# Kernel tuning notes

Hardware: AMD Instinct MI355X
Metric: run time of the kernel (lower is better)

## Reference

```python
import jax, jax.numpy as jnp
import numpy as np
from jax import lax


def _lstm_cell(x, h, c, W_ih, W_hh, b_ih, b_hh):
    # torch nn.LSTMCell: gates = x W_ih^T + b_ih + h W_hh^T + b_hh, order i,f,g,o
    gates = x @ W_ih.T + h @ W_hh.T + (b_ih + b_hh)
    i, f, g, o = jnp.split(gates, 4, axis=-1)
    c_new = jax.nn.sigmoid(f) * c + jax.nn.sigmoid(i) * jnp.tanh(g)
    h_new = jax.nn.sigmoid(o) * jnp.tanh(c_new)
    return h_new, c_new


def setup_inputs():
    key = jax.random.key(0)
    ks = jax.random.split(key, 10)
    B, S, E, H, V = 128, 20, 512, 512, 10000
    images = jax.random.normal(ks[0], (B, E), jnp.float32)
    captions = jax.random.randint(ks[1], (B, S), 0, V)
    length = jax.random.randint(ks[2], (B, 1), 2, S + 1)
    length = length.at[0, 0].set(S)  # guarantee max decode length == S-1 (static shape)
    s = 0.05
    emb = jax.random.normal(ks[3], (V, E), jnp.float32) * s
    W_ih = jax.random.normal(ks[4], (4 * H, E), jnp.float32) * s
    W_hh = jax.random.normal(ks[5], (4 * H, H), jnp.float32) * s
    b_ih = jax.random.normal(ks[6], (4 * H,), jnp.float32) * s
    b_hh = jax.random.normal(ks[7], (4 * H,), jnp.float32) * s
    fc_w = jax.random.normal(ks[8], (V, H), jnp.float32) * s
    fc_b = jax.random.normal(ks[9], (V,), jnp.float32) * s
    return dict(images=images, captions=captions, length=length, emb=emb,
                W_ih=W_ih, W_hh=W_hh, b_ih=b_ih, b_hh=b_hh, fc_w=fc_w, fc_b=fc_b)


def reference(images, captions, length, emb, W_ih, W_hh, b_ih, b_hh, fc_w, fc_b):
    B, S = captions.shape
    T = S - 1  # static max(decode_lengths) by construction
    H = W_hh.shape[1]
    lens = length[:, 0]
    sort_ind = jnp.argsort(-lens)  # stable descending sort, like torch .sort(descending=True)
    sorted_lens = lens[sort_ind]
    dec_len = sorted_lens - 1
    features = images[sort_ind]
    captions_s = captions[sort_ind]
    embeddings = emb[captions_s]  # [B, S, E]

    zeros = jnp.zeros((B, H), images.dtype)
    h, c = _lstm_cell(features, zeros, zeros, W_ih, W_hh, b_ih, b_hh)

    xs = (jnp.swapaxes(embeddings[:, :T, :], 0, 1), jnp.arange(T))  # [T,B,E], [T]

    def step(carry, x):
        h, c = carry
        x_t, t = x
        # ragged batch in the original == masking here: rows with dec_len<=t never
        # contribute to any future valid output (lengths sorted descending).
        h, c = _lstm_cell(x_t, h, c, W_ih, W_hh, b_ih, b_hh)
        preds = h @ fc_w.T + fc_b  # dropout is identity in eval mode
        preds = jnp.where((dec_len > t)[:, None], preds, 0.0)
        return (h, c), preds

    (_, _), preds = lax.scan(step, (h, c), xs)
    predictions = jnp.swapaxes(preds, 0, 1)  # [B, T, V]
    return predictions, captions_s, dec_len, sort_ind
```

## Files before the change

### kernel.cpp

```cpp
#include <hip/hip_runtime.h>

typedef float  f32x4 __attribute__((ext_vector_type(4)));
typedef short  s16x8 __attribute__((ext_vector_type(8)));
typedef unsigned short u16x4 __attribute__((ext_vector_type(4)));

#define MFMA16(a,b,c) __builtin_amdgcn_mfma_f32_16x16x32_bf16(a,b,c,0,0,0)

#define PRED_ELEMS 24320000ull

__device__ __forceinline__ unsigned short f2bf(float f){
  unsigned u = __builtin_bit_cast(unsigned, f);
  u += 0x7fffu + ((u >> 16) & 1u);
  return (unsigned short)(u >> 16);
}
__device__ __forceinline__ float sigf(float x){ return 1.0f/(1.0f + __expf(-x)); }
__device__ __forceinline__ float tanh_(float x){
  x = fminf(15.0f, fmaxf(-15.0f, x));
  float e = __expf(2.0f*x);
  return (e - 1.0f) / (e + 1.0f);
}
__device__ __forceinline__ s16x8 ld8(const unsigned short* p){
  return *reinterpret_cast<const s16x8*>(p);
}
__device__ __forceinline__ void gload_lds16(const unsigned short* src, unsigned short* dst){
  __builtin_amdgcn_global_load_lds(
      (const __attribute__((address_space(1))) void*)src,
      (__attribute__((address_space(3))) void*)dst, 16, 0, 0);
}

__global__ void k0_sort(const int* __restrict__ length, const int* __restrict__ captions,
                        float* __restrict__ out, int* __restrict__ sortp,
                        int* __restrict__ nactp, unsigned int* __restrict__ cnt4k)
{
  __shared__ int sl[128], sdl[128], ssi[128];
  int tid = threadIdx.x;
  for (int k = tid; k < 1024; k += 128) cnt4k[k] = 0u;
  if (tid < 128) sl[tid] = length[tid];
  __syncthreads();
  if (tid < 128){
    int l = sl[tid];
    int rank = 0;
    for (int j = 0; j < 128; ++j){
      int lj = sl[j];
      rank += (lj > l) || (lj == l && j < tid);
    }
    sortp[rank] = tid;
    ssi[rank] = tid;   sdl[rank] = l - 1;
  }
  __syncthreads();
  if (tid < 20){
    int c = 0;
    for (int r = 0; r < 128; ++r) c += (sdl[r] >= tid);
    nactp[tid] = c;
  }
  if (tid < 128){
    const size_t P = PRED_ELEMS;
    int si = ssi[tid];
    for (int t = 0; t < 20; ++t) out[P + tid*20 + t] = (float)captions[si*20 + t];
    out[P + 2560 + tid] = (float)sdl[tid];
    out[P + 2688 + tid] = (float)si;
  }
}

__device__ __forceinline__ void cvt4(unsigned short* dst, const float* src, int u){
  f32x4 v = *reinterpret_cast<const f32x4*>(src + (size_t)u*4);
  u16x4 o;
  o[0]=f2bf(v[0]); o[1]=f2bf(v[1]); o[2]=f2bf(v[2]); o[3]=f2bf(v[3]);
  *reinterpret_cast<u16x4*>(dst + (size_t)u*4) = o;
}

__global__ void k1_convert(const float* __restrict__ images, const int* __restrict__ captions,
    const float* __restrict__ emb, const float* __restrict__ wih, const float* __restrict__ whh,
    const float* __restrict__ bih, const float* __restrict__ bhh, const float* __restrict__ fcw,
    const int* __restrict__ sortp,
    unsigned short* __restrict__ wihb, unsigned short* __restrict__ whhb,
    unsigned short* __restrict__ fcwb, float* __restrict__ biasp,
    unsigned short* __restrict__ xseq, unsigned short* __restrict__ hseq,
    unsigned short* __restrict__ hloc)
{
  const int U0 = 262144;
  const int U1 = 262144;
  const int U2 = 1294336;
  const int U3 = 512;
  const int U4 = 327680;
  const int U5 = 16384;
  const int U6 = 16384;
  const int total = U0+U1+U2+U3+U4+U5+U6;
  for (int i = blockIdx.x*blockDim.x + threadIdx.x; i < total; i += gridDim.x*blockDim.x){
    int j = i;
    if (j < U0){ cvt4(wihb, wih, j); continue; }
    j -= U0;
    if (j < U1){ cvt4(whhb, whh, j); continue; }
    j -= U1;
    if (j < U2){
      int row = j >> 7;
      if (row < 10000) cvt4(fcwb, fcw, j);
      else { u16x4 z = {0,0,0,0}; *reinterpret_cast<u16x4*>(fcwb + (size_t)j*4) = z; }
      continue;
    }
    j -= U2;
    if (j < U3){
      int e0 = j*4;
      for (int e = 0; e < 4; ++e) biasp[e0+e] = bih[e0+e] + bhh[e0+e];
      continue;
    }
    j -= U3;
    if (j < U4){
      int elem = j*4;
      int s = elem >> 16;
      int rem = elem & 65535;
      int r = rem >> 9;
      int k = rem & 511;
      const float* src;
      if (s == 0) src = images + (size_t)sortp[r]*512 + k;
      else {
        int cap = captions[sortp[r]*20 + (s-1)];
        src = emb + (size_t)cap*512 + k;
      }
      f32x4 v = *reinterpret_cast<const f32x4*>(src);
      u16x4 o;
      o[0]=f2bf(v[0]); o[1]=f2bf(v[1]); o[2]=f2bf(v[2]); o[3]=f2bf(v[3]);
      *reinterpret_cast<u16x4*>(xseq + (size_t)j*4) = o;
      continue;
    }
    j -= U4;
    if (j < U5){ u16x4 z = {0,0,0,0}; *reinterpret_cast<u16x4*>(hseq + (size_t)j*4) = z; continue; }
    j -= U5;
    {
      int e0 = j*4;
      int x = e0 >> 13;
      int rem = e0 & 8191;
      u16x4 z = {0,0,0,0};
      *reinterpret_cast<u16x4*>(hloc + (size_t)x*172032 + rem) = z;
    }
  }
}

__global__ __launch_bounds__(256) void lstm_chain(
    const unsigned short* __restrict__ xseq, const unsigned short* __restrict__ wih,
    const unsigned short* __restrict__ whh, const float* __restrict__ biasp,
    unsigned short* __restrict__ hseq, unsigned short* __restrict__ hloc,
    const int* __restrict__ nact, unsigned int* __restrict__ claimc,
    unsigned int* __restrict__ flags)
{
  const int tid = threadIdx.x;
  __shared__ int s_xw;
  __shared__ unsigned short WIl[64*524];
  __shared__ unsigned short WHl[64*524];
  __shared__ float pg[4][4][16][17];

  if (tid == 0){
    unsigned xcc;
    asm volatile("s_getreg_b32 %0, hwreg(20, 0, 4)" : "=s"(xcc));
    int x = (int)(xcc & 7u);
    unsigned slot = __hip_atomic_fetch_add(claimc + x*64, 1u,
                      __ATOMIC_RELAXED, __HIP_MEMORY_SCOPE_AGENT);
    s_xw = (x << 8) | (int)(slot & 255u);
  }
  __syncthreads();
  const int x = s_xw >> 8;
  const int w = s_xw & 255;
  if (w >= 32) return;
  const int R0 = x*16;
  const int C0 = w*16;
  unsigned int* myflags = flags + x*64;

  const int lane = tid & 63;
  const int kk   = tid >> 6;
  const int fr   = lane & 15;
  const int fkq  = (lane >> 4) * 8;

  for (int idx = tid; idx < 64*64; idx += 256){
    int lr = idx >> 6, kc = (idx & 63)*8;
    int q = lr >> 4, jj = lr & 15;
    size_t off = (size_t)(q*512 + C0 + jj)*512 + kc;
    *reinterpret_cast<s16x8*>(&WIl[lr*524 + kc]) = ld8(wih + off);
    *reinterpret_cast<s16x8*>(&WHl[lr*524 + kc]) = ld8(whh + off);
  }

  unsigned short* hl = hloc + (size_t)x*172032;
  const int prow = tid >> 4;
  const int pcol = tid & 15;
  const float bz0 = biasp[       C0 + pcol];
  const float bz1 = biasp[ 512 + C0 + pcol];
  const float bz2 = biasp[1024 + C0 + pcol];
  const float bz3 = biasp[1536 + C0 + pcol];
  float creg = 0.f;

  s16x8 ax[4];
  #pragma unroll
  for (int i = 0; i < 4; ++i)
    ax[i] = ld8(xseq + (R0 + fr)*512 + kk*128 + i*32 + fkq);
  __syncthreads();

  for (int s = 0; s < 20; ++s){
    if (R0 >= nact[s]) break;
    const unsigned short* hp = hl + (size_t)s*8192;

    s16x8 ah[4];
    #pragma unroll
    for (int i = 0; i < 4; ++i)
      ah[i] = ld8(hp + fr*512 + kk*128 + i*32 + fkq);

    #pragma unroll
    for (int q = 0; q < 4; ++q){
      f32x4 accx = (f32x4){0.f,0.f,0.f,0.f};
      f32x4 acch = (f32x4){0.f,0.f,0.f,0.f};
      #pragma unroll
      for (int i = 0; i < 4; ++i){
        s16x8 bi = *reinterpret_cast<const s16x8*>(&WIl[(q*16 + fr)*524 + kk*128 + i*32 + fkq]);
        accx = MFMA16(ax[i], bi, accx);
      }
      #pragma unroll
      for (int i = 0; i < 4; ++i){
        s16x8 bh = *reinterpret_cast<const s16x8*>(&WHl[(q*16 + fr)*524 + kk*128 + i*32 + fkq]);
        acch = MFMA16(ah[i], bh, acch);
      }
      const int rr = (lane >> 4) * 4;
      #pragma unroll
      for (int p = 0; p < 4; ++p)
        pg[kk][q][rr + p][fr] = accx[p] + acch[p];
    }
    __syncthreads();

    unsigned short hb;
    {
      float iv = pg[0][0][prow][pcol] + pg[1][0][prow][pcol]
               + pg[2][0][prow][pcol] + pg[3][0][prow][pcol] + bz0;
      float fv = pg[0][1][prow][pcol] + pg[1][1][prow][pcol]
               + pg[2][1][prow][pcol] + pg[3][1][prow][pcol] + bz1;
      float gv = pg[0][2][prow][pcol] + pg[1][2][prow][pcol]
               + pg[2][2][prow][pcol] + pg[3][2][prow][pcol] + bz2;
      float ov = pg[0][3][prow][pcol] + pg[1][3][prow][pcol]
               + pg[2][3][prow][pcol] + pg[3][3][prow][pcol] + bz3;
      creg = sigf(fv)*creg + sigf(iv)*tanh_(gv);
      float h = sigf(ov)*tanh_(creg);
      hb = f2bf(h);
      hl[(size_t)(s+1)*8192 + prow*512 + C0 + pcol] = hb;
    }
    __syncthreads();

    hseq[(size_t)(s+1)*65536 + (R0 + prow)*512 + C0 + pcol] = hb;

    if (s < 19 && nact[s+1] > R0){
      const unsigned tgt = (unsigned)(s + 1);
      const unsigned short* xp = xseq + (size_t)(s+1)*65536;
      #pragma unroll
      for (int i = 0; i < 4; ++i)
        ax[i] = ld8(xp + (R0 + fr)*512 + kk*128 + i*32 + fkq);

      if (tid == 0){
        unsigned int* fa = myflags + w;
        asm volatile("global_atomic_swap %0, %1, off"
                     :: "v"(fa), "v"(tgt) : "memory");
      }
      if (tid < 64){
        unsigned int* pa = myflags + (tid & 31);
        long guard = 0;
        for (;;){
          bool ok = true;
          if (tid < 32){
            unsigned old;
            asm volatile("global_atomic_add %0, %1, %2, off sc0\n\t"
                         "s_waitcnt vmcnt(0)"
                         : "=v"(old) : "v"(pa), "v"(0u) : "memory");
            ok = (old >= tgt);
          }
          if (__all(ok) || ++guard > (1L << 20)) break;
          __builtin_amdgcn_s_sleep(1);
        }
      }
      __syncthreads();
    }
  }
}

__global__ __launch_bounds__(256) void fc_kernel(
    const unsigned short* __restrict__ hseq, const unsigned short* __restrict__ fcwb,
    const float* __restrict__ fcb, const int* __restrict__ nact,
    float* __restrict__ out)
{
  const int b    = blockIdx.x;
  const int x    = b & 7;
  const int slot = b >> 3;
  const int t    = slot % 19;
  const int p    = x + 8*(slot/19);
  if (p >= 79) return;
  const int v0   = p * 128;
  const int tid  = threadIdx.x;

  __shared__ unsigned short Ab[2][128*64];
  __shared__ unsigned short Bb[2][128*64];

  const unsigned short* Ag = hseq + (size_t)(t + 2)*65536;
  const unsigned short* Bg = fcwb + (size_t)v0*512;
  const int n_t = nact[t + 1];

  const int srow = tid >> 3;
  const int sphy = tid & 7;
  const int wuni = (tid >> 6) << 9;

  #define STAGE(gsrc, lbuf, kt)                                              \
    _Pragma("unroll")                                                        \
    for (int call = 0; call < 4; ++call){                                    \
      int row_ = call*32 + srow;                                             \
      gload_lds16(gsrc + (size_t)row_*512 + (kt)*64 + ((sphy ^ (row_ & 7)) << 3), \
                  lbuf + call*2048 + wuni);                                  \
    }

  const int lane = tid & 63;
  const int wv   = tid >> 6;
  const int wr   = wv >> 1, wc = wv & 1;
  const int fr   = lane & 15;
  const int hi   = lane >> 4;

  f32x4 acc[4][4];
  #pragma unroll
  for (int i = 0; i < 4; ++i)
    #pragma unroll
    for (int j = 0; j < 4; ++j)
      acc[i][j] = (f32x4){0.f,0.f,0.f,0.f};

  STAGE(Ag, Ab[0], 0)
  STAGE(Bg, Bb[0], 0)
  asm volatile("s_waitcnt vmcnt(0)" ::: "memory");
  __syncthreads();

  int cur = 0;
  for (int kt = 0; kt < 8; ++kt){
    if (kt < 7){
      STAGE(Ag, Ab[cur^1], kt+1)
      STAGE(Bg, Bb[cur^1], kt+1)
    }
    const unsigned short* As = Ab[cur];
    const unsigned short* Bs = Bb[cur];
    #pragma unroll
    for (int kk = 0; kk < 2; ++kk){
      const int c = kk*4 + hi;
      s16x8 af[4], bf[4];
      #pragma unroll
      for (int i = 0; i < 4; ++i){
        int row = wr*64 + i*16 + fr;
        af[i] = ld8(As + row*64 + ((c ^ (row & 7)) << 3));
      }
      #pragma unroll
      for (int j = 0; j < 4; ++j){
        int col = wc*64 + j*16 + fr;
        bf[j] = ld8(Bs + col*64 + ((c ^ (col & 7)) << 3));
      }
      #pragma unroll
      for (int i = 0; i < 4; ++i)
        #pragma unroll
        for (int j = 0; j < 4; ++j)
          acc[i][j] = MFMA16(af[i], bf[j], acc[i][j]);
    }
    asm volatile("s_waitcnt vmcnt(0)" ::: "memory");
    __syncthreads();
    cur ^= 1;
  }

  const int rr = hi * 4;
  #pragma unroll
  for (int j = 0; j < 4; ++j){
    int v = v0 + wc*64 + j*16 + fr;
    if (v >= 10000) continue;
    float bb = fcb[v];
    #pragma unroll
    for (int i = 0; i < 4; ++i){
      #pragma unroll
      for (int pp = 0; pp < 4; ++pp){
        int r = wr*64 + i*16 + rr + pp;
        out[(size_t)(r*19 + t)*10000 + v] = (r < n_t) ? (acc[i][j][pp] + bb) : 0.0f;
      }
    }
  }
  #undef STAGE
}

extern "C" void kernel_launch(void* const* d_in, const int* in_sizes, int n_in,
                              void* d_out, int out_size, void* d_ws, size_t ws_size,
                              hipStream_t stream) {
  const float* images   = (const float*)d_in[0];
  const int*   captions = (const int*)  d_in[1];
  const int*   length   = (const int*)  d_in[2];
  const float* emb      = (const float*)d_in[3];
  const float* W_ih     = (const float*)d_in[4];
  const float* W_hh     = (const float*)d_in[5];
  const float* b_ih     = (const float*)d_in[6];
  const float* b_hh     = (const float*)d_in[7];
  const float* fc_w     = (const float*)d_in[8];
  const float* fc_b     = (const float*)d_in[9];
  float* out = (float*)d_out;
  char*  ws  = (char*)d_ws;

  int*            sortp  = (int*)           (ws + 0);
  int*            nactp  = (int*)           (ws + 2048);
  float*          biasp  = (float*)         (ws + 4096);
  unsigned int*   cnt4k  = (unsigned int*)  (ws + 12288);
  unsigned int*   claimc = cnt4k;
  unsigned int*   flags  = cnt4k + 512;
  unsigned short* hloc   = (unsigned short*)(ws + 16384);
  unsigned short* hseq   = (unsigned short*)(ws + 2768896);
  unsigned short* xseq   = (unsigned short*)(ws + 5521408);
  unsigned short* wihb   = (unsigned short*)(ws + 8142848);
  unsigned short* whhb   = (unsigned short*)(ws + 10240000);
  unsigned short* fcwb   = (unsigned short*)(ws + 12337152);

  k0_sort<<<1, 128, 0, stream>>>(length, captions, out, sortp, nactp, cnt4k);
  k1_convert<<<4096, 256, 0, stream>>>(images, captions, emb, W_ih, W_hh, b_ih, b_hh,
                                       fc_w, sortp, wihb, whhb, fcwb, biasp, xseq, hseq, hloc);
  lstm_chain<<<256, 256, 0, stream>>>(xseq, wihb, whhb, biasp, hseq, hloc,
                                      nactp, claimc, flags);
  fc_kernel<<<1520, 256, 0, stream>>>(hseq, fcwb, fc_b, nactp, out);
}
```

Before: 143.2 us.

## Keep LSTM weights in registers and precompute input projection off critical path

The per-block W_ih/W_hh slices move from LDS into registers (32 s16x8 fragments per thread). The x·W_ih product for the next step is now computed before the cross-block barrier wait rather than after it, leaving only h·W_hh on the serial recurrence path. The flag store and poll switch from inline-asm atomics to HIP atomic store and load, and a 50KB LDS pad plus launch_bounds(…,1) force one block per CU. The cost is heavy VGPR pressure and possible spilling, and relaxed atomic loads may change the visibility guarantees of the spin-wait.

```diff
diff --git a/kernel.cpp b/kernel.cpp
--- a/kernel.cpp
+++ b/kernel.cpp
@@ -136,7 +136,7 @@
   }
 }
 
-__global__ __launch_bounds__(256) void lstm_chain(
+__global__ __launch_bounds__(256, 1) void lstm_chain(
     const unsigned short* __restrict__ xseq, const unsigned short* __restrict__ wih,
     const unsigned short* __restrict__ whh, const float* __restrict__ biasp,
     unsigned short* __restrict__ hseq, unsigned short* __restrict__ hloc,
@@ -145,9 +145,10 @@
 {
   const int tid = threadIdx.x;
   __shared__ int s_xw;
-  __shared__ unsigned short WIl[64*524];
-  __shared__ unsigned short WHl[64*524];
-  __shared__ float pg[4][4][16][17];
+  __shared__ float pgh[4][4][16][17];
+  __shared__ float pgx[4][4][16][17];
+  __shared__ unsigned char lds_pad[51200];
+  asm volatile("" : : "v"(&lds_pad[tid & 127]) : "memory");
 
   if (tid == 0){
     unsigned xcc;
@@ -169,14 +170,17 @@
   const int kk   = tid >> 6;
   const int fr   = lane & 15;
   const int fkq  = (lane >> 4) * 8;
-
-  for (int idx = tid; idx < 64*64; idx += 256){
-    int lr = idx >> 6, kc = (idx & 63)*8;
-    int q = lr >> 4, jj = lr & 15;
-    size_t off = (size_t)(q*512 + C0 + jj)*512 + kc;
-    *reinterpret_cast<s16x8*>(&WIl[lr*524 + kc]) = ld8(wih + off);
-    *reinterpret_cast<s16x8*>(&WHl[lr*524 + kc]) = ld8(whh + off);
-  }
+  const int rr   = (lane >> 4) * 4;
+
+  s16x8 BI[4][4], BH[4][4];
+  #pragma unroll
+  for (int q = 0; q < 4; ++q)
+    #pragma unroll
+    for (int i = 0; i < 4; ++i){
+      size_t off = (size_t)(q*512 + C0 + fr)*512 + kk*128 + i*32 + fkq;
+      BI[q][i] = ld8(wih + off);
+      BH[q][i] = ld8(whh + off);
+    }
 
   unsigned short* hl = hloc + (size_t)x*172032;
   const int prow = tid >> 4;
@@ -187,10 +191,22 @@
   const float bz3 = biasp[1536 + C0 + pcol];
   float creg = 0.f;
 
-  s16x8 ax[4];
-  #pragma unroll
-  for (int i = 0; i < 4; ++i)
-    ax[i] = ld8(xseq + (R0 + fr)*512 + kk*128 + i*32 + fkq);
+  {
+    s16x8 ax[4];
+    #pragma unroll
+    for (int i = 0; i < 4; ++i)
+      ax[i] = ld8(xseq + (R0 + fr)*512 + kk*128 + i*32 + fkq);
+    #pragma unroll
+    for (int q = 0; q < 4; ++q){
+      f32x4 accx = (f32x4){0.f,0.f,0.f,0.f};
+      #pragma unroll
+      for (int i = 0; i < 4; ++i)
+        accx = MFMA16(ax[i], BI[q][i], accx);
+      #pragma unroll
+      for (int p = 0; p < 4; ++p)
+        pgx[kk][q][rr + p][fr] = accx[p];
+    }
+  }
   __syncthreads();
 
   for (int s = 0; s < 20; ++s){
@@ -201,38 +217,36 @@
     #pragma unroll
     for (int i = 0; i < 4; ++i)
       ah[i] = ld8(hp + fr*512 + kk*128 + i*32 + fkq);
-
     #pragma unroll
     for (int q = 0; q < 4; ++q){
-      f32x4 accx = (f32x4){0.f,0.f,0.f,0.f};
       f32x4 acch = (f32x4){0.f,0.f,0.f,0.f};
       #pragma unroll
-      for (int i = 0; i < 4; ++i){
-        s16x8 bi = *reinterpret_cast<const s16x8*>(&WIl[(q*16 + fr)*524 + kk*128 + i*32 + fkq]);
-        accx = MFMA16(ax[i], bi, accx);
-      }
-      #pragma unroll
-      for (int i = 0; i < 4; ++i){
-        s16x8 bh = *reinterpret_cast<const s16x8*>(&WHl[(q*16 + fr)*524 + kk*128 + i*32 + fkq]);
-        acch = MFMA16(ah[i], bh, acch);
-      }
-      const int rr = (lane >> 4) * 4;
+      for (int i = 0; i < 4; ++i)
+        acch = MFMA16(ah[i], BH[q][i], acch);
       #pragma unroll
       for (int p = 0; p < 4; ++p)
-        pg[kk][q][rr + p][fr] = accx[p] + acch[p];
+        pgh[kk][q][rr + p][fr] = acch[p];
     }
     __syncthreads();
 
     unsigned short hb;
     {
-      float iv = pg[0][0][prow][pcol] + pg[1][0][prow][pcol]
-               + pg[2][0][prow][pcol] + pg[3][0][prow][pcol] + bz0;
-      float fv = pg[0][1][prow][pcol] + pg[1][1][prow][pcol]
-               + pg[2][1][prow][pcol] + pg[3][1][prow][pcol] + bz1;
-      float gv = pg[0][2][prow][pcol] + pg[1][2][prow][pcol]
-               + pg[2][2][prow][pcol] + pg[3][2][prow][pcol] + bz2;
-      float ov = pg[0][3][prow][pcol] + pg[1][3][prow][pcol]
-               + pg[2][3][prow][pcol] + pg[3][3][prow][pcol] + bz3;
+      float iv = pgh[0][0][prow][pcol] + pgh[1][0][prow][pcol]
+               + pgh[2][0][prow][pcol] + pgh[3][0][prow][pcol]
+               + pgx[0][0][prow][pcol] + pgx[1][0][prow][pcol]
+               + pgx[2][0][prow][pcol] + pgx[3][0][prow][pcol] + bz0;
+      float fv = pgh[0][1][prow][pcol] + pgh[1][1][prow][pcol]
+               + pgh[2][1][prow][pcol] + pgh[3][1][prow][pcol]
+               + pgx[0][1][prow][pcol] + pgx[1][1][prow][pcol]
+               + pgx[2][1][prow][pcol] + pgx[3][1][prow][pcol] + bz1;
+      float gv = pgh[0][2][prow][pcol] + pgh[1][2][prow][pcol]
+               + pgh[2][2][prow][pcol] + pgh[3][2][prow][pcol]
+               + pgx[0][2][prow][pcol] + pgx[1][2][prow][pcol]
+               + pgx[2][2][prow][pcol] + pgx[3][2][prow][pcol] + bz2;
+      float ov = pgh[0][3][prow][pcol] + pgh[1][3][prow][pcol]
+               + pgh[2][3][prow][pcol] + pgh[3][3][prow][pcol]
+               + pgx[0][3][prow][pcol] + pgx[1][3][prow][pcol]
+               + pgx[2][3][prow][pcol] + pgx[3][3][prow][pcol] + bz3;
       creg = sigf(fv)*creg + sigf(iv)*tanh_(gv);
       float h = sigf(ov)*tanh_(creg);
       hb = f2bf(h);
@@ -244,28 +258,34 @@
 
     if (s < 19 && nact[s+1] > R0){
       const unsigned tgt = (unsigned)(s + 1);
-      const unsigned short* xp = xseq + (size_t)(s+1)*65536;
-      #pragma unroll
-      for (int i = 0; i < 4; ++i)
-        ax[i] = ld8(xp + (R0 + fr)*512 + kk*128 + i*32 + fkq);
-
-      if (tid == 0){
-        unsigned int* fa = myflags + w;
-        asm volatile("global_atomic_swap %0, %1, off"
-                     :: "v"(fa), "v"(tgt) : "memory");
-      }
+      if (tid == 0)
+        __hip_atomic_store(&myflags[w], tgt, __ATOMIC_RELAXED, __HIP_MEMORY_SCOPE_AGENT);
+
+      {
+        const unsigned short* xp = xseq + (size_t)(s+1)*65536;
+        s16x8 ax[4];
+        #pragma unroll
+        for (int i = 0; i < 4; ++i)
+          ax[i] = ld8(xp + (R0 + fr)*512 + kk*128 + i*32 + fkq);
+        #pragma unroll
+        for (int q = 0; q < 4; ++q){
+          f32x4 accx = (f32x4){0.f,0.f,0.f,0.f};
+          #pragma unroll
+          for (int i = 0; i < 4; ++i)
+            accx = MFMA16(ax[i], BI[q][i], accx);
+          #pragma unroll
+          for (int p = 0; p < 4; ++p)
+            pgx[kk][q][rr + p][fr] = accx[p];
+        }
+      }
+
       if (tid < 64){
-        unsigned int* pa = myflags + (tid & 31);
         long guard = 0;
         for (;;){
           bool ok = true;
-          if (tid < 32){
-            unsigned old;
-            asm volatile("global_atomic_add %0, %1, %2, off sc0\n\t"
-                         "s_waitcnt vmcnt(0)"
-                         : "=v"(old) : "v"(pa), "v"(0u) : "memory");
-            ok = (old >= tgt);
-          }
+          if (tid < 32)
+            ok = (__hip_atomic_load(&myflags[tid], __ATOMIC_RELAXED,
+                                    __HIP_MEMORY_SCOPE_AGENT) >= tgt);
           if (__all(ok) || ++guard > (1L << 20)) break;
           __builtin_amdgcn_s_sleep(1);
         }
```

Result: faster. 122.9 us (-14.2%).
